# Optimization experiments

Hardware: AMD Instinct MI355X
Metric: run time of the kernel (lower is better)

## Reference

```python
import jax, jax.numpy as jnp
import numpy as np

D_IN, D_OUT, NUM_HEADS, TOP_K = 512, 512, 8, 32
D_HEAD = D_OUT // NUM_HEADS


def setup_inputs() -> dict:
    key = jax.random.key(0)
    ks = jax.random.split(key, 9)
    s_in = 1.0 / np.sqrt(D_IN)
    s_out = 1.0 / np.sqrt(D_OUT)
    return {
        "x": jax.random.normal(ks[0], (8, 1024, D_IN), dtype=jnp.float32),
        # weights stored as (d_in, d_out) so y = x @ W + b (same math as torch Linear)
        "Wq": jax.random.uniform(ks[1], (D_IN, D_OUT), jnp.float32, -s_in, s_in),
        "bq": jax.random.uniform(ks[2], (D_OUT,), jnp.float32, -s_in, s_in),
        "Wk": jax.random.uniform(ks[3], (D_IN, D_OUT), jnp.float32, -s_in, s_in),
        "bk": jax.random.uniform(ks[4], (D_OUT,), jnp.float32, -s_in, s_in),
        "Wv": jax.random.uniform(ks[5], (D_IN, D_OUT), jnp.float32, -s_in, s_in),
        "bv": jax.random.uniform(ks[6], (D_OUT,), jnp.float32, -s_in, s_in),
        "Wo": jax.random.uniform(ks[7], (D_OUT, D_OUT), jnp.float32, -s_out, s_out),
        "bo": jax.random.uniform(ks[8], (D_OUT,), jnp.float32, -s_out, s_out),
    }


def reference(x, Wq, bq, Wk, bk, Wv, bv, Wo, bo):
    B, N, _ = x.shape
    H, Dh = NUM_HEADS, D_HEAD

    def split_heads(t):  # [B,N,d_out] -> [B,H,N,Dh]
        return t.reshape(B, N, H, Dh).transpose(0, 2, 1, 3)

    q = split_heads(x @ Wq + bq)
    k = split_heads(x @ Wk + bk)
    v = split_heads(x @ Wv + bv)

    scores = jnp.einsum("bhnd,bhmd->bhnm", q, k) / np.sqrt(Dh).astype(np.float32)

    k_eff = min(TOP_K, N)
    topk_vals, topk_idx = jax.lax.top_k(scores, k_eff)  # [B,H,N,k]

    # scatter top-k values into a -inf mask along the last axis
    bi = jnp.arange(B)[:, None, None, None]
    hi = jnp.arange(H)[None, :, None, None]
    ni = jnp.arange(N)[None, None, :, None]
    mask = jnp.full_like(scores, -jnp.inf)
    mask = mask.at[bi, hi, ni, topk_idx].set(topk_vals)

    attn = jax.nn.softmax(mask, axis=-1)
    out = jnp.einsum("bhnm,bhmd->bhnd", attn, v)
    out = out.transpose(0, 2, 1, 3).reshape(B, N, H * Dh)
    return out @ Wo + bo
```

## Files before the change

### kernel.cpp

```cpp
#include <hip/hip_runtime.h>
#include <math.h>
#include <stdint.h>


#define MAXREC 2048
#define GWIN 6.0e-6f

__device__ inline int wave_sum16(int cc) {
  int tot = 0;
#pragma unroll
  for (int bit = 0; bit < 5; bit++)
    tot += ((int)__popcll(__ballot(((cc >> bit) & 1) != 0))) << bit;
  return tot;
}

__device__ inline float bf16rnd(float x) {
  unsigned u = __float_as_uint(x);
  u = (u + 0x7FFFu + ((u >> 16) & 1u)) & 0xFFFF0000u;
  return __uint_as_float(u);
}

__device__ inline float bf16ulp(float a) {
  unsigned e = (__float_as_uint(a) >> 23) & 0xFFu;
  if (e < 9u) e = 9u;
  return __uint_as_float((e - 8u) << 23);
}

__global__ __launch_bounds__(256) void qkv_gemm(const float* __restrict__ X,
                                                const float* __restrict__ Wq, const float* __restrict__ bq,
                                                const float* __restrict__ Wk, const float* __restrict__ bk,
                                                const float* __restrict__ Wv, const float* __restrict__ bv,
                                                float* __restrict__ Qf, float* __restrict__ KfT,
                                                float* __restrict__ Vo) {
  __shared__ float Xs[16][132];
  __shared__ float Ws[3][16][68];
  const int tid = threadIdx.x;
  const int tx = tid & 15;
  const int ty8 = (tid >> 4) * 8;
  const int c0 = blockIdx.x * 64;
  const int m0 = blockIdx.y * 128;
  const int mW = tid >> 2;
  const int kk4 = (tid & 3) * 4;
  const int wkk = tid >> 4;
  const int wcol = (tid & 15) * 4;

  float acc[3][8][4] = {};
  float4 xr0, xr1, wr0, wr1, wr2;

#define LOAD_REGS(K0)                                                              \
  {                                                                                \
    xr0 = *(const float4*)&X[(size_t)(m0 + mW) * 512 + (K0) + kk4];                \
    xr1 = *(const float4*)&X[(size_t)(m0 + 64 + mW) * 512 + (K0) + kk4];           \
    wr0 = *(const float4*)&Wq[(size_t)((K0) + wkk) * 512 + c0 + wcol];             \
    wr1 = *(const float4*)&Wk[(size_t)((K0) + wkk) * 512 + c0 + wcol];             \
    wr2 = *(const float4*)&Wv[(size_t)((K0) + wkk) * 512 + c0 + wcol];             \
  }

  LOAD_REGS(0);
  for (int k0 = 0; k0 < 512; k0 += 16) {
    Xs[kk4 + 0][mW] = xr0.x; Xs[kk4 + 1][mW] = xr0.y;
    Xs[kk4 + 2][mW] = xr0.z; Xs[kk4 + 3][mW] = xr0.w;
    Xs[kk4 + 0][mW + 64] = xr1.x; Xs[kk4 + 1][mW + 64] = xr1.y;
    Xs[kk4 + 2][mW + 64] = xr1.z; Xs[kk4 + 3][mW + 64] = xr1.w;
    *(float4*)&Ws[0][wkk][wcol] = wr0;
    *(float4*)&Ws[1][wkk][wcol] = wr1;
    *(float4*)&Ws[2][wkk][wcol] = wr2;
    __syncthreads();
    if (k0 + 16 < 512) LOAD_REGS(k0 + 16);
#pragma unroll
    for (int kk = 0; kk < 16; kk++) {
      float4 xa = *(const float4*)&Xs[kk][ty8];
      float4 xb = *(const float4*)&Xs[kk][ty8 + 4];
      float xr[8] = {xa.x, xa.y, xa.z, xa.w, xb.x, xb.y, xb.z, xb.w};
#pragma unroll
      for (int p = 0; p < 3; p++) {
        float4 b4 = *(const float4*)&Ws[p][kk][tx * 4];
        float br[4] = {b4.x, b4.y, b4.z, b4.w};
#pragma unroll
        for (int i = 0; i < 8; i++)
#pragma unroll
          for (int j = 0; j < 4; j++)
            acc[p][i][j] = fmaf(xr[i], br[j], acc[p][i][j]);
      }
    }
    __syncthreads();
  }
#undef LOAD_REGS
#pragma unroll
  for (int i = 0; i < 8; i++) {
    int m = m0 + ty8 + i;
    int bb = m >> 10, nn = m & 1023;
#pragma unroll
    for (int j = 0; j < 4; j++) {
      int c = c0 + tx * 4 + j;
      Qf[(size_t)m * 512 + c] = acc[0][i][j] + bq[c];
      KfT[((size_t)bb * 512 + c) * 1024 + nn] = acc[1][i][j] + bk[c];
      Vo[(size_t)m * 512 + c] = acc[2][i][j] + bv[c];
    }
  }
}

__global__ __launch_bounds__(256) void gemm_out(const float* __restrict__ X,
                                                const float* __restrict__ W,
                                                const float* __restrict__ bias,
                                                float* __restrict__ out) {
  __shared__ float Xs[16][132];
  __shared__ float Ws[16][68];
  const int tid = threadIdx.x;
  const int tx = tid & 15;
  const int ty8 = (tid >> 4) * 8;
  const int c0 = blockIdx.x * 64;
  const int m0 = blockIdx.y * 128;
  const int mW = tid >> 2;
  const int kk4 = (tid & 3) * 4;
  const int wkk = tid >> 4;
  const int wcol = (tid & 15) * 4;

  float acc[8][4] = {};
  float4 xr0, xr1, wr0;

#define LOAD_REGS(K0)                                                              \
  {                                                                                \
    xr0 = *(const float4*)&X[(size_t)(m0 + mW) * 512 + (K0) + kk4];                \
    xr1 = *(const float4*)&X[(size_t)(m0 + 64 + mW) * 512 + (K0) + kk4];           \
    wr0 = *(const float4*)&W[(size_t)((K0) + wkk) * 512 + c0 + wcol];              \
  }

  LOAD_REGS(0);
  for (int k0 = 0; k0 < 512; k0 += 16) {
    Xs[kk4 + 0][mW] = xr0.x; Xs[kk4 + 1][mW] = xr0.y;
    Xs[kk4 + 2][mW] = xr0.z; Xs[kk4 + 3][mW] = xr0.w;
    Xs[kk4 + 0][mW + 64] = xr1.x; Xs[kk4 + 1][mW + 64] = xr1.y;
    Xs[kk4 + 2][mW + 64] = xr1.z; Xs[kk4 + 3][mW + 64] = xr1.w;
    *(float4*)&Ws[wkk][wcol] = wr0;
    __syncthreads();
    if (k0 + 16 < 512) LOAD_REGS(k0 + 16);
#pragma unroll
    for (int kk = 0; kk < 16; kk++) {
      float4 xa = *(const float4*)&Xs[kk][ty8];
      float4 xb = *(const float4*)&Xs[kk][ty8 + 4];
      float xr[8] = {xa.x, xa.y, xa.z, xa.w, xb.x, xb.y, xb.z, xb.w};
      float4 b4 = *(const float4*)&Ws[kk][tx * 4];
      float br[4] = {b4.x, b4.y, b4.z, b4.w};
#pragma unroll
      for (int i = 0; i < 8; i++)
#pragma unroll
        for (int j = 0; j < 4; j++)
          acc[i][j] = fmaf(xr[i], br[j], acc[i][j]);
    }
    __syncthreads();
  }
#undef LOAD_REGS
#pragma unroll
  for (int i = 0; i < 8; i++) {
    int m = m0 + ty8 + i;
#pragma unroll
    for (int j = 0; j < 4; j++) {
      int c = c0 + tx * 4 + j;
      out[(size_t)m * 512 + c] = acc[i][j] + bias[c];
    }
  }
}

template <int RR>
__device__ __forceinline__ void row_tail(const float (&acc)[4][16], float smax, float tH, int cH,
                                         int lane, int w, int b, int n0, int h,
                                         const float* __restrict__ vb,
                                         float* __restrict__ AO,
                                         int* __restrict__ cnt, int* __restrict__ recs,
                                         float (&swp)[16][32], int (&smp)[16][32]) {
  const int need = 32 - cH;

  unsigned int sel = 0;
#pragma unroll
  for (int j = 0; j < 16; j++) sel |= (acc[RR][j] >= tH) ? (1u << j) : 0u;

  float s_a = INFINITY; int ma = -1;
  for (int e = 0; e < need; e++) {
    float bv = -INFINITY; int bm = 0x7fffffff;
#pragma unroll
    for (int j = 0; j < 16; j++)
      if (!(sel & (1u << j))) {
        int m = ((j >> 2) << 8) + 4 * lane + (j & 3);
        if (acc[RR][j] > bv || (acc[RR][j] == bv && m < bm)) { bv = acc[RR][j]; bm = m; }
      }
    for (int off_ = 32; off_ >= 1; off_ >>= 1) {
      float ov = __shfl_xor(bv, off_, 64); int om = __shfl_xor(bm, off_, 64);
      if (ov > bv || (ov == bv && om < bm)) { bv = ov; bm = om; }
    }
    if (lane == ((bm >> 2) & 63)) sel |= 1u << (((bm >> 8) << 2) | (bm & 3));
    s_a = bv; ma = bm;
  }

  float s_r; int mr;
  {
    float bv = -INFINITY; int bm = 0x7fffffff;
#pragma unroll
    for (int j = 0; j < 16; j++)
      if (!(sel & (1u << j))) {
        int m = ((j >> 2) << 8) + 4 * lane + (j & 3);
        if (acc[RR][j] > bv || (acc[RR][j] == bv && m < bm)) { bv = acc[RR][j]; bm = m; }
      }
    for (int off_ = 32; off_ >= 1; off_ >>= 1) {
      float ov = __shfl_xor(bv, off_, 64); int om = __shfl_xor(bm, off_, 64);
      if (ov > bv || (ov == bv && om < bm)) { bv = ov; bm = om; }
    }
    s_r = bv; mr = bm;
  }

  bool maybe = (tH - s_r < GWIN);
  if (maybe && need == 0) {
    float bv = INFINITY; int bm = -1;
#pragma unroll
    for (int j = 0; j < 16; j++)
      if (sel & (1u << j)) {
        int m = ((j >> 2) << 8) + 4 * lane + (j & 3);
        if (acc[RR][j] < bv || (acc[RR][j] == bv && m > bm)) { bv = acc[RR][j]; bm = m; }
      }
    for (int off_ = 32; off_ >= 1; off_ >>= 1) {
      float ov = __shfl_xor(bv, off_, 64); int om = __shfl_xor(bm, off_, 64);
      if (ov < bv || (ov == bv && om > bm)) { bv = ov; bm = om; }
    }
    s_a = bv; ma = bm;
  }

  const int rowi = w * 4 + RR;
  float zp = 0.f;
  int base = 0;
#pragma unroll
  for (int j = 0; j < 16; j++) {
    unsigned long long bm64 = __ballot(((sel >> j) & 1) != 0);
    if ((sel >> j) & 1) {
      int pos = base + __popcll(bm64 & ((1ull << lane) - 1ull));
      float wgt = __expf(acc[RR][j] - smax);
      swp[rowi][pos] = wgt;
      smp[rowi][pos] = ((j >> 2) << 8) + 4 * lane + (j & 3);
      zp += wgt;
    }
    base += __popcll(bm64);
  }
  float Z = zp;
#pragma unroll
  for (int off_ = 32; off_ >= 1; off_ >>= 1) Z += __shfl_xor(Z, off_, 64);

  if (maybe && (s_a - s_r) < GWIN && lane == 0) {
    int idx = atomicAdd(cnt, 1);
    if (idx < MAXREC) {
      int* rec = recs + idx * 8;
      rec[0] = b * 1024 + n0 + rowi;
      rec[1] = h;
      rec[2] = ma;
      rec[3] = mr;
      ((float*)rec)[4] = __expf(s_a - smax);
      ((float*)rec)[5] = __expf(s_r - smax);
      ((float*)rec)[6] = Z;
      rec[7] = 0;
    }
  }

  __builtin_amdgcn_wave_barrier();
  asm volatile("s_waitcnt lgkmcnt(0)" ::: "memory");
  __builtin_amdgcn_wave_barrier();

  float o0 = 0.f, o1 = 0.f, o2 = 0.f, o3 = 0.f;
#pragma unroll
  for (int tt = 0; tt < 32; tt += 4) {
    float w0 = swp[rowi][tt], w1 = swp[rowi][tt + 1];
    float w2 = swp[rowi][tt + 2], w3 = swp[rowi][tt + 3];
    int m0_ = smp[rowi][tt], m1_ = smp[rowi][tt + 1];
    int m2_ = smp[rowi][tt + 2], m3_ = smp[rowi][tt + 3];
    o0 = fmaf(w0, vb[(size_t)m0_ * 512], o0);
    o1 = fmaf(w1, vb[(size_t)m1_ * 512], o1);
    o2 = fmaf(w2, vb[(size_t)m2_ * 512], o2);
    o3 = fmaf(w3, vb[(size_t)m3_ * 512], o3);
  }
  AO[(size_t)(b * 1024 + n0 + rowi) * 512 + h * 64 + lane] = ((o0 + o1) + (o2 + o3)) / Z;
}

template <int R0, int R1>
__device__ __forceinline__ void process_pair(const float (&acc)[4][16],
                                             int lane, int w, int b, int n0, int h,
                                             const float* __restrict__ vb,
                                             float* __restrict__ AO,
                                             int* __restrict__ cnt, int* __restrict__ recs,
                                             float (&swp)[16][32], int (&smp)[16][32]) {
  float s1a = 0.f, s2a = 0.f, mxa = -INFINITY;
  float s1b = 0.f, s2b = 0.f, mxb = -INFINITY;
#pragma unroll
  for (int j = 0; j < 16; j++) {
    float a = acc[R0][j], bb = acc[R1][j];
    s1a += a; s2a = fmaf(a, a, s2a); mxa = fmaxf(mxa, a);
    s1b += bb; s2b = fmaf(bb, bb, s2b); mxb = fmaxf(mxb, bb);
  }
#pragma unroll
  for (int off_ = 32; off_ >= 1; off_ >>= 1) {
    s1a += __shfl_xor(s1a, off_, 64);
    s2a += __shfl_xor(s2a, off_, 64);
    mxa = fmaxf(mxa, __shfl_xor(mxa, off_, 64));
    s1b += __shfl_xor(s1b, off_, 64);
    s2b += __shfl_xor(s2b, off_, 64);
    mxb = fmaxf(mxb, __shfl_xor(mxb, off_, 64));
  }
  const float mua = s1a * (1.f / 1024.f);
  const float sga = sqrtf(fmaxf(s2a * (1.f / 1024.f) - mua * mua, 1e-20f));
  const float mub = s1b * (1.f / 1024.f);
  const float sgb = sqrtf(fmaxf(s2b * (1.f / 1024.f) - mub * mub, 1e-20f));

  float tLa = -INFINITY, tHa = INFINITY, tca = fmaf(1.92f, sga, mua);
  float tLb = -INFINITY, tHb = INFINITY, tcb = fmaf(1.92f, sgb, mub);
  int cHa = 0, cHb = 0;
  bool dna = false, dnb = false;
  for (int it = 0; it < 4; it++) {
    int cca = 0, ccb = 0;
    if (!dna) {
      int ccl = 0;
#pragma unroll
      for (int j = 0; j < 16; j++) ccl += (acc[R0][j] >= tca) ? 1 : 0;
      cca = wave_sum16(ccl);
    }
    if (!dnb) {
      int ccl = 0;
#pragma unroll
      for (int j = 0; j < 16; j++) ccl += (acc[R1][j] >= tcb) ? 1 : 0;
      ccb = wave_sum16(ccl);
    }
    if (!dna) {
      if (cca > 32) {
        tLa = tca;
      } else {
        tHa = tca; cHa = cca;
        if (cca >= 26) dna = true;
      }
      if (!dna) {
        float z = (tca - mua) / sga;
        float pdf = 0.39894228f * __expf(-0.5f * z * z);
        float tn = tca - (float)(29 - cca) * sga / (1024.f * pdf);
        if (!(tn > tLa) || !(tn < tHa)) {
          if (tLa == -INFINITY) tn = tca - 4.f * sga;
          else if (tHa == INFINITY) tn = tca + 4.f * sga;
          else tn = 0.5f * (tLa + tHa);
        }
        tca = tn;
      }
    }
    if (!dnb) {
      if (ccb > 32) {
        tLb = tcb;
      } else {
        tHb = tcb; cHb = ccb;
        if (ccb >= 26) dnb = true;
      }
      if (!dnb) {
        float z = (tcb - mub) / sgb;
        float pdf = 0.39894228f * __expf(-0.5f * z * z);
        float tn = tcb - (float)(29 - ccb) * sgb / (1024.f * pdf);
        if (!(tn > tLb) || !(tn < tHb)) {
          if (tLb == -INFINITY) tn = tcb - 4.f * sgb;
          else if (tHb == INFINITY) tn = tcb + 4.f * sgb;
          else tn = 0.5f * (tLb + tHb);
        }
        tcb = tn;
      }
    }
    if (dna && dnb) break;
  }

  row_tail<R0>(acc, mxa, tHa, cHa, lane, w, b, n0, h, vb, AO, cnt, recs, swp, smp);
  row_tail<R1>(acc, mxb, tHb, cHb, lane, w, b, n0, h, vb, AO, cnt, recs, swp, smp);
}

__global__ __launch_bounds__(256) void attn_topk(const float* __restrict__ Qf,
                                                 const float* __restrict__ KfT,
                                                 const float* __restrict__ V,
                                                 float* __restrict__ AO,
                                                 int* __restrict__ cnt,
                                                 int* __restrict__ recs) {
  __shared__ float qp[4][64][4];
  __shared__ float swp[16][32];
  __shared__ int smp[16][32];

  const int tid = threadIdx.x;
  const int lane = tid & 63;
  const int w = tid >> 6;
  const int rb = blockIdx.x * 16;
  const int b = rb >> 13;
  const int h = (rb >> 10) & 7;
  const int n0 = rb & 1023;

#pragma unroll
  for (int it = 0; it < 4; it++) {
    int idx = tid + it * 256;
    int row = idx >> 6, d = idx & 63;
    qp[row >> 2][d][row & 3] = Qf[(size_t)(b * 1024 + n0 + row) * 512 + h * 64 + d];
  }
  __syncthreads();

  float acc[4][16];
#pragma unroll
  for (int r = 0; r < 4; r++)
#pragma unroll
    for (int j = 0; j < 16; j++) acc[r][j] = 0.f;

  const float* kbase = KfT + ((size_t)b * 512 + h * 64) * 1024 + 4 * lane;

#pragma unroll 2
  for (int d = 0; d < 64; d++) {
    const float* kd = kbase + (size_t)d * 1024;
    float4 kv4[4];
#pragma unroll
    for (int c = 0; c < 4; c++) kv4[c] = *(const float4*)&kd[c * 256];
    float4 qv4 = *(const float4*)&qp[w][d][0];
    float qv[4] = {qv4.x, qv4.y, qv4.z, qv4.w};
#pragma unroll
    for (int c = 0; c < 4; c++) {
      float kv[4] = {kv4[c].x, kv4[c].y, kv4[c].z, kv4[c].w};
#pragma unroll
      for (int r = 0; r < 4; r++)
#pragma unroll
        for (int e = 0; e < 4; e++)
          acc[r][c * 4 + e] = fmaf(qv[r], kv[e], acc[r][c * 4 + e]);
    }
  }

#pragma unroll
  for (int r = 0; r < 4; r++)
#pragma unroll
    for (int j = 0; j < 16; j++) acc[r][j] *= 0.125f;

  const float* vb = V + (size_t)b * 1024 * 512 + h * 64 + lane;

  process_pair<0, 1>(acc, lane, w, b, n0, h, vb, AO, cnt, recs, swp, smp);
  process_pair<2, 3>(acc, lane, w, b, n0, h, vb, AO, cnt, recs, swp, smp);
}

__global__ __launch_bounds__(256) void fixup(const float* __restrict__ AO,
                                             const float* __restrict__ V,
                                             const float* __restrict__ Wo,
                                             float* __restrict__ out,
                                             const int* __restrict__ cnt,
                                             const int* __restrict__ recs) {
  __shared__ float dsh[64];
  __shared__ int keys[MAXREC];
  __shared__ short order[MAXREC];
  const int tid = threadIdx.x;
  int count = *cnt;
  if (count > MAXREC) count = MAXREC;

  for (int i = tid; i < count; i += 256) keys[i] = recs[i * 8] * 8 + recs[i * 8 + 1];
  __syncthreads();
  for (int i = tid; i < count; i += 256) {
    int ki = keys[i], rank = 0;
    for (int j = 0; j < count; j++) rank += (keys[j] < ki) ? 1 : 0;
    order[rank] = (short)i;
  }
  __syncthreads();

  for (int r = 0; r < count; r++) {
    const int* rec = recs + (int)order[r] * 8;
    const int gr = rec[0], h = rec[1], ma = rec[2], mr = rec[3];
    const float wa = ((const float*)rec)[4];
    const float wr = ((const float*)rec)[5];
    const float Z = ((const float*)rec)[6];
    const int bb = gr >> 10;

    if (tid < 64) {
      float ao = AO[(size_t)gr * 512 + h * 64 + tid];
      float va = V[(size_t)(bb * 1024 + ma) * 512 + h * 64 + tid];
      float vr = V[(size_t)(bb * 1024 + mr) * 512 + h * 64 + tid];
      float aor = (ao * Z - wa * va + wr * vr) / (Z - wa + wr);
      dsh[tid] = ao - aor;
    }
    __syncthreads();

    {
      const int col = tid;
      const float* wob = Wo + (size_t)h * 64 * 512;
      float t0 = 0.f, t1 = 0.f;
#pragma unroll
      for (int d0 = 0; d0 < 64; d0 += 8) {
        float dv[8], w0[8], w1[8];
#pragma unroll
        for (int e = 0; e < 8; e++) {
          dv[e] = dsh[d0 + e];
          w0[e] = wob[(size_t)(d0 + e) * 512 + col];
          w1[e] = wob[(size_t)(d0 + e) * 512 + col + 256];
        }
#pragma unroll
        for (int e = 0; e < 8; e++) {
          t0 = fmaf(dv[e], w0[e], t0);
          t1 = fmaf(dv[e], w1[e], t1);
        }
      }
#pragma unroll
      for (int half = 0; half < 2; half++) {
        int c = col + half * 256;
        float tt = half ? t1 : t0;
        float ya = out[(size_t)gr * 512 + c];
        float yr = ya - tt;
        float A = bf16rnd(ya), R = bf16rnd(yr);
        float span = fabsf(A - R);
        float ulp = fmaxf(bf16ulp(A), bf16ulp(R));
        if (0.5f * span + 0.5f * ulp <= 0.00800f) {
          out[(size_t)gr * 512 + c] = 0.5f * (A + R);
        }
      }
    }
    __syncthreads();
  }
}

extern "C" void kernel_launch(void* const* d_in, const int* in_sizes, int n_in,
                              void* d_out, int out_size, void* d_ws, size_t ws_size,
                              hipStream_t stream) {
  const float* x = (const float*)d_in[0];
  const float* Wq = (const float*)d_in[1];
  const float* bq = (const float*)d_in[2];
  const float* Wk = (const float*)d_in[3];
  const float* bk = (const float*)d_in[4];
  const float* Wv = (const float*)d_in[5];
  const float* bv = (const float*)d_in[6];
  const float* Wo = (const float*)d_in[7];
  const float* bo = (const float*)d_in[8];
  float* out = (float*)d_out;

  char* ws = (char*)d_ws;
  float* Qf = (float*)(ws);
  float* KfT = (float*)(ws + (size_t)16777216);
  float* V = (float*)(ws + (size_t)33554432);
  float* AO = (float*)(ws + (size_t)50331648);
  int* cnt = (int*)(ws + (size_t)67108864);
  int* recs = (int*)(ws + (size_t)67108864 + 256);

  hipMemsetAsync(cnt, 0, 4, stream);

  hipLaunchKernelGGL(qkv_gemm, dim3(8, 64), dim3(256), 0, stream,
                     x, Wq, bq, Wk, bk, Wv, bv, Qf, KfT, V);
  hipLaunchKernelGGL(attn_topk, dim3(4096), dim3(256), 0, stream, Qf, KfT, V, AO, cnt, recs);
  hipLaunchKernelGGL(gemm_out, dim3(8, 64), dim3(256), 0, stream, AO, Wo, bo, out);
  hipLaunchKernelGGL(fixup, dim3(1), dim3(256), 0, stream, AO, V, Wo, out, cnt, recs);
}
```

Before: 536.5 us.

## Use packed 64-bit keys for top-k argmax and retune threshold search

Replaces the float-plus-index argmax loops in the top-k selection tail with single 64-bit monotone keys (value bits high, inverted index low), so each compare and shuffle step handles one packed key. Weights and byte offsets are packed into one int2 shared array to halve LDS reads in the gather. The Newton threshold search is retuned to a different initial z, target count and acceptance cutoff, aiming for fewer serial extraction iterations. Launch bounds hint two blocks per CU. The 64-bit compares and shuffles may cost more registers, and the retuned threshold can trigger more fallback iterations.

```diff
diff --git a/kernel.cpp b/kernel.cpp
--- a/kernel.cpp
+++ b/kernel.cpp
@@ -12,6 +12,14 @@
   for (int bit = 0; bit < 5; bit++)
     tot += ((int)__popcll(__ballot(((cc >> bit) & 1) != 0))) << bit;
   return tot;
+}
+
+__device__ inline unsigned mono32(float x) {
+  unsigned u = __float_as_uint(x);
+  return (u & 0x80000000u) ? ~u : (u | 0x80000000u);
+}
+__device__ inline float unmono32(unsigned k) {
+  return (k & 0x80000000u) ? __uint_as_float(k & 0x7FFFFFFFu) : __uint_as_float(~k);
 }
 
 __device__ inline float bf16rnd(float x) {
@@ -168,60 +176,69 @@
                                          const float* __restrict__ vb,
                                          float* __restrict__ AO,
                                          int* __restrict__ cnt, int* __restrict__ recs,
-                                         float (&swp)[16][32], int (&smp)[16][32]) {
+                                         int2 (&spk)[16][32]) {
   const int need = 32 - cH;
 
+  unsigned long long pk[16];
+#pragma unroll
+  for (int j = 0; j < 16; j++) {
+    int m = ((j >> 2) << 8) + 4 * lane + (j & 3);
+    pk[j] = ((unsigned long long)mono32(acc[RR][j]) << 32) | (unsigned)(~m);
+  }
+
   unsigned int sel = 0;
 #pragma unroll
   for (int j = 0; j < 16; j++) sel |= (acc[RR][j] >= tH) ? (1u << j) : 0u;
 
-  float s_a = INFINITY; int ma = -1;
+  unsigned long long ka = ~0ull;
   for (int e = 0; e < need; e++) {
-    float bv = -INFINITY; int bm = 0x7fffffff;
-#pragma unroll
-    for (int j = 0; j < 16; j++)
-      if (!(sel & (1u << j))) {
-        int m = ((j >> 2) << 8) + 4 * lane + (j & 3);
-        if (acc[RR][j] > bv || (acc[RR][j] == bv && m < bm)) { bv = acc[RR][j]; bm = m; }
-      }
+    unsigned long long bk = 0ull;
+#pragma unroll
+    for (int j = 0; j < 16; j++) {
+      unsigned long long cand = ((sel >> j) & 1u) ? 0ull : pk[j];
+      bk = (cand > bk) ? cand : bk;
+    }
+#pragma unroll
     for (int off_ = 32; off_ >= 1; off_ >>= 1) {
-      float ov = __shfl_xor(bv, off_, 64); int om = __shfl_xor(bm, off_, 64);
-      if (ov > bv || (ov == bv && om < bm)) { bv = ov; bm = om; }
-    }
-    if (lane == ((bm >> 2) & 63)) sel |= 1u << (((bm >> 8) << 2) | (bm & 3));
-    s_a = bv; ma = bm;
-  }
-
-  float s_r; int mr;
-  {
-    float bv = -INFINITY; int bm = 0x7fffffff;
-#pragma unroll
-    for (int j = 0; j < 16; j++)
-      if (!(sel & (1u << j))) {
-        int m = ((j >> 2) << 8) + 4 * lane + (j & 3);
-        if (acc[RR][j] > bv || (acc[RR][j] == bv && m < bm)) { bv = acc[RR][j]; bm = m; }
-      }
+      unsigned long long ok = __shfl_xor(bk, off_, 64);
+      bk = (ok > bk) ? ok : bk;
+    }
+    int m = (int)(~(unsigned)bk);
+    if (lane == ((m >> 2) & 63)) sel |= 1u << (((m >> 8) << 2) | (m & 3));
+    ka = bk;
+  }
+  float s_a = unmono32((unsigned)(ka >> 32));
+  int ma = (int)(~(unsigned)ka);
+
+  unsigned long long bk = 0ull;
+#pragma unroll
+  for (int j = 0; j < 16; j++) {
+    unsigned long long cand = ((sel >> j) & 1u) ? 0ull : pk[j];
+    bk = (cand > bk) ? cand : bk;
+  }
+#pragma unroll
+  for (int off_ = 32; off_ >= 1; off_ >>= 1) {
+    unsigned long long ok = __shfl_xor(bk, off_, 64);
+    bk = (ok > bk) ? ok : bk;
+  }
+  const float s_r = unmono32((unsigned)(bk >> 32));
+  const int mr = (int)(~(unsigned)bk);
+
+  bool maybe = (need > 0) ? ((s_a - s_r) < GWIN) : ((tH - s_r) < GWIN);
+  if (maybe && need == 0) {
+    unsigned long long mk = ~0ull;
+#pragma unroll
+    for (int j = 0; j < 16; j++) {
+      unsigned long long cand = ((sel >> j) & 1u) ? pk[j] : ~0ull;
+      mk = (cand < mk) ? cand : mk;
+    }
+#pragma unroll
     for (int off_ = 32; off_ >= 1; off_ >>= 1) {
-      float ov = __shfl_xor(bv, off_, 64); int om = __shfl_xor(bm, off_, 64);
-      if (ov > bv || (ov == bv && om < bm)) { bv = ov; bm = om; }
-    }
-    s_r = bv; mr = bm;
-  }
-
-  bool maybe = (tH - s_r < GWIN);
-  if (maybe && need == 0) {
-    float bv = INFINITY; int bm = -1;
-#pragma unroll
-    for (int j = 0; j < 16; j++)
-      if (sel & (1u << j)) {
-        int m = ((j >> 2) << 8) + 4 * lane + (j & 3);
-        if (acc[RR][j] < bv || (acc[RR][j] == bv && m > bm)) { bv = acc[RR][j]; bm = m; }
-      }
-    for (int off_ = 32; off_ >= 1; off_ >>= 1) {
-      float ov = __shfl_xor(bv, off_, 64); int om = __shfl_xor(bm, off_, 64);
-      if (ov < bv || (ov == bv && om > bm)) { bv = ov; bm = om; }
-    }
-    s_a = bv; ma = bm;
+      unsigned long long ok = __shfl_xor(mk, off_, 64);
+      mk = (ok < mk) ? ok : mk;
+    }
+    s_a = unmono32((unsigned)(mk >> 32));
+    ma = (int)(~(unsigned)mk);
   }
 
   const int rowi = w * 4 + RR;
@@ -232,9 +249,9 @@
     unsigned long long bm64 = __ballot(((sel >> j) & 1) != 0);
     if ((sel >> j) & 1) {
       int pos = base + __popcll(bm64 & ((1ull << lane) - 1ull));
+      int m = ((j >> 2) << 8) + 4 * lane + (j & 3);
       float wgt = __expf(acc[RR][j] - smax);
-      swp[rowi][pos] = wgt;
-      smp[rowi][pos] = ((j >> 2) << 8) + 4 * lane + (j & 3);
+      spk[rowi][pos] = make_int2(m << 11, __float_as_int(wgt));
       zp += wgt;
     }
     base += __popcll(bm64);
@@ -262,17 +279,16 @@
   asm volatile("s_waitcnt lgkmcnt(0)" ::: "memory");
   __builtin_amdgcn_wave_barrier();
 
+  const char* vbb = (const char*)vb;
   float o0 = 0.f, o1 = 0.f, o2 = 0.f, o3 = 0.f;
 #pragma unroll
   for (int tt = 0; tt < 32; tt += 4) {
-    float w0 = swp[rowi][tt], w1 = swp[rowi][tt + 1];
-    float w2 = swp[rowi][tt + 2], w3 = swp[rowi][tt + 3];
-    int m0_ = smp[rowi][tt], m1_ = smp[rowi][tt + 1];
-    int m2_ = smp[rowi][tt + 2], m3_ = smp[rowi][tt + 3];
-    o0 = fmaf(w0, vb[(size_t)m0_ * 512], o0);
-    o1 = fmaf(w1, vb[(size_t)m1_ * 512], o1);
-    o2 = fmaf(w2, vb[(size_t)m2_ * 512], o2);
-    o3 = fmaf(w3, vb[(size_t)m3_ * 512], o3);
+    int2 p0 = spk[rowi][tt], p1 = spk[rowi][tt + 1];
+    int2 p2 = spk[rowi][tt + 2], p3 = spk[rowi][tt + 3];
+    o0 = fmaf(__int_as_float(p0.y), *(const float*)(vbb + p0.x), o0);
+    o1 = fmaf(__int_as_float(p1.y), *(const float*)(vbb + p1.x), o1);
+    o2 = fmaf(__int_as_float(p2.y), *(const float*)(vbb + p2.x), o2);
+    o3 = fmaf(__int_as_float(p3.y), *(const float*)(vbb + p3.x), o3);
   }
   AO[(size_t)(b * 1024 + n0 + rowi) * 512 + h * 64 + lane] = ((o0 + o1) + (o2 + o3)) / Z;
 }
@@ -283,7 +299,7 @@
                                              const float* __restrict__ vb,
                                              float* __restrict__ AO,
                                              int* __restrict__ cnt, int* __restrict__ recs,
-                                             float (&swp)[16][32], int (&smp)[16][32]) {
+                                             int2 (&spk)[16][32]) {
   float s1a = 0.f, s2a = 0.f, mxa = -INFINITY;
   float s1b = 0.f, s2b = 0.f, mxb = -INFINITY;
 #pragma unroll
@@ -306,8 +322,8 @@
   const float mub = s1b * (1.f / 1024.f);
   const float sgb = sqrtf(fmaxf(s2b * (1.f / 1024.f) - mub * mub, 1e-20f));
 
-  float tLa = -INFINITY, tHa = INFINITY, tca = fmaf(1.92f, sga, mua);
-  float tLb = -INFINITY, tHb = INFINITY, tcb = fmaf(1.92f, sgb, mub);
+  float tLa = -INFINITY, tHa = INFINITY, tca = fmaf(1.875f, sga, mua);
+  float tLb = -INFINITY, tHb = INFINITY, tcb = fmaf(1.875f, sgb, mub);
   int cHa = 0, cHb = 0;
   bool dna = false, dnb = false;
   for (int it = 0; it < 4; it++) {
@@ -329,12 +345,12 @@
         tLa = tca;
       } else {
         tHa = tca; cHa = cca;
-        if (cca >= 26) dna = true;
+        if (cca >= 29) dna = true;
       }
       if (!dna) {
         float z = (tca - mua) / sga;
         float pdf = 0.39894228f * __expf(-0.5f * z * z);
-        float tn = tca - (float)(29 - cca) * sga / (1024.f * pdf);
+        float tn = tca - (float)(31 - cca) * sga / (1024.f * pdf);
         if (!(tn > tLa) || !(tn < tHa)) {
           if (tLa == -INFINITY) tn = tca - 4.f * sga;
           else if (tHa == INFINITY) tn = tca + 4.f * sga;
@@ -348,12 +364,12 @@
         tLb = tcb;
       } else {
         tHb = tcb; cHb = ccb;
-        if (ccb >= 26) dnb = true;
+        if (ccb >= 29) dnb = true;
       }
       if (!dnb) {
         float z = (tcb - mub) / sgb;
         float pdf = 0.39894228f * __expf(-0.5f * z * z);
-        float tn = tcb - (float)(29 - ccb) * sgb / (1024.f * pdf);
+        float tn = tcb - (float)(31 - ccb) * sgb / (1024.f * pdf);
         if (!(tn > tLb) || !(tn < tHb)) {
           if (tLb == -INFINITY) tn = tcb - 4.f * sgb;
           else if (tHb == INFINITY) tn = tcb + 4.f * sgb;
@@ -365,19 +381,18 @@
     if (dna && dnb) break;
   }
 
-  row_tail<R0>(acc, mxa, tHa, cHa, lane, w, b, n0, h, vb, AO, cnt, recs, swp, smp);
-  row_tail<R1>(acc, mxb, tHb, cHb, lane, w, b, n0, h, vb, AO, cnt, recs, swp, smp);
-}
-
-__global__ __launch_bounds__(256) void attn_topk(const float* __restrict__ Qf,
-                                                 const float* __restrict__ KfT,
-                                                 const float* __restrict__ V,
-                                                 float* __restrict__ AO,
-                                                 int* __restrict__ cnt,
-                                                 int* __restrict__ recs) {
+  row_tail<R0>(acc, mxa, tHa, cHa, lane, w, b, n0, h, vb, AO, cnt, recs, spk);
+  row_tail<R1>(acc, mxb, tHb, cHb, lane, w, b, n0, h, vb, AO, cnt, recs, spk);
+}
+
+__global__ __launch_bounds__(256, 2) void attn_topk(const float* __restrict__ Qf,
+                                                    const float* __restrict__ KfT,
+                                                    const float* __restrict__ V,
+                                                    float* __restrict__ AO,
+                                                    int* __restrict__ cnt,
+                                                    int* __restrict__ recs) {
   __shared__ float qp[4][64][4];
-  __shared__ float swp[16][32];
-  __shared__ int smp[16][32];
+  __shared__ int2 spk[16][32];
 
   const int tid = threadIdx.x;
   const int lane = tid & 63;
@@ -429,8 +444,8 @@
 
   const float* vb = V + (size_t)b * 1024 * 512 + h * 64 + lane;
 
-  process_pair<0, 1>(acc, lane, w, b, n0, h, vb, AO, cnt, recs, swp, smp);
-  process_pair<2, 3>(acc, lane, w, b, n0, h, vb, AO, cnt, recs, swp, smp);
+  process_pair<0, 1>(acc, lane, w, b, n0, h, vb, AO, cnt, recs, spk);
+  process_pair<2, 3>(acc, lane, w, b, n0, h, vb, AO, cnt, recs, spk);
 }
 
 __global__ __launch_bounds__(256) void fixup(const float* __restrict__ AO,
```

After: 695.9 us. 1.3x slower.
